# Optimization experiments

Measured on AMD Instinct MI355X. Metric: run time of the kernel, lower is better.

Reference implementation:

```python
import jax, jax.numpy as jnp
import numpy as np

N = 50000
E = 1600000
F_IN = 128
MP_UNITS = [32, 32, 32, 32, 16, 16, 16, 16, 8, 8, 8, 8]
MLP_UNITS = [16, 16]
DELTA = 2.0


def _lin(k, fi, fo):
    kw, kb = jax.random.split(k)
    s = 1.0 / np.sqrt(fi)
    W = jax.random.uniform(kw, (fi, fo), minval=-s, maxval=s, dtype=jnp.float32)
    b = jax.random.uniform(kb, (fo,), minval=-s, maxval=s, dtype=jnp.float32)
    return W, b


def setup_inputs() -> dict:
    key = jax.random.key(0)
    ks = jax.random.split(key, 64)
    inp = {}
    inp['x'] = jax.random.normal(ks[0], (N, F_IN), dtype=jnp.float32)
    inp['edge_index'] = jax.random.randint(ks[1], (2, E), 0, N, dtype=jnp.int32)
    inp['edge_weight'] = jax.random.uniform(ks[2], (E,), dtype=jnp.float32)
    inp['Wi'], inp['bi'] = _lin(ks[3], F_IN, F_IN)
    d = F_IN
    for i, u in enumerate(MP_UNITS):
        inp['Wc%d' % i], inp['bc%d' % i] = _lin(ks[4 + i], d, u)
        d = u
    for i, u in enumerate(MLP_UNITS):
        inp['Wm%d' % i], inp['bm%d' % i] = _lin(ks[20 + i], d, u)
        d = u
    inp['Wf'], inp['bf'] = _lin(ks[30], d, 1)
    return inp


def reference(x, edge_index, edge_weight, Wi, bi,
              Wc0, bc0, Wc1, bc1, Wc2, bc2, Wc3, bc3, Wc4, bc4, Wc5, bc5,
              Wc6, bc6, Wc7, bc7, Wc8, bc8, Wc9, bc9, Wc10, bc10, Wc11, bc11,
              Wm0, bm0, Wm1, bm1, Wf, bf):
    n = x.shape[0]
    src, dst = edge_index[0], edge_index[1]
    # delta_gcn_matrix: P = (1-delta) I + delta * D^{-1/2} A D^{-1/2}
    deg = jax.ops.segment_sum(edge_weight, dst, num_segments=n)
    dinv = jnp.where(deg > 0, jax.lax.rsqrt(jnp.maximum(deg, 1e-12)), 0.0)
    w = DELTA * dinv[src] * edge_weight * dinv[dst]  # [E]
    self_w = 1.0 - DELTA

    h = x @ Wi + bi

    def conv(h, W, b):
        hw = h @ W                                        # [N, out]
        msg = hw[src] * w[:, None]                        # gather + scale [E, out]
        agg = jax.ops.segment_sum(msg, dst, num_segments=n)  # scatter-add
        return agg + self_w * hw + b                      # fold in self-loops

    convs = [(Wc0, bc0), (Wc1, bc1), (Wc2, bc2), (Wc3, bc3), (Wc4, bc4), (Wc5, bc5),
             (Wc6, bc6), (Wc7, bc7), (Wc8, bc8), (Wc9, bc9), (Wc10, bc10), (Wc11, bc11)]
    for W, b in convs:
        h = jnp.tanh(conv(h, W, b))
    for W, b in [(Wm0, bm0), (Wm1, bm1)]:
        h = jax.nn.relu(h @ W + b)
    return jnp.tanh(h @ Wf + bf)  # [N, 1]
```

## Files before the change

### kernel.cpp

```cpp
#include <hip/hip_runtime.h>


constexpr int kN = 50000;
constexpr int kE = 1600000;
constexpr float kSelfW = -1.0f;
constexpr int kCAP = 72;
constexpr int PAD_N = 50048;
constexpr int kPROWS = PAD_N / 8;
constexpr int E4  = kE / 4;
constexpr int E4B = (E4 + 255) / 256;
constexpr int NBG = (kN + 255) / 256;
constexpr int WSN = 50016;

typedef int      v4i __attribute__((ext_vector_type(4)));
typedef float    v4f __attribute__((ext_vector_type(4)));
typedef _Float16 h8v __attribute__((ext_vector_type(8)));

__device__ __forceinline__ int rowmap(int r) {
  return (r & 7) * kPROWS + (r >> 3);
}
__device__ __forceinline__ unsigned packcw(int col, float w) {
  _Float16 h = (_Float16)w;
  unsigned short u;
  __builtin_memcpy(&u, &h, 2);
  return (unsigned)(unsigned short)col | ((unsigned)u << 16);
}
__device__ __forceinline__ float unpw(unsigned e) {
  unsigned short u = (unsigned short)(e >> 16);
  _Float16 h;
  __builtin_memcpy(&h, &u, 2);
  return (float)h;
}
__device__ __forceinline__ unsigned pack2h(float a, float b) {
  _Float16 ha = (_Float16)a, hb = (_Float16)b;
  unsigned short ua, ub;
  __builtin_memcpy(&ua, &ha, 2);
  __builtin_memcpy(&ub, &hb, 2);
  return (unsigned)ua | ((unsigned)ub << 16);
}
__device__ __forceinline__ float fast_tanh(float x) {
  float t = __expf(2.0f * x);
  float r = __builtin_amdgcn_rcpf(t + 1.0f);
  return 1.0f - 2.0f * r;
}

__global__ __launch_bounds__(256)
void prep(int* __restrict__ cnt, const float* __restrict__ Wi,
          const float* __restrict__ bi, const float* __restrict__ Wc0,
          float* __restrict__ Weff, float* __restrict__ beff) {
  if (blockIdx.x < 49) {
    int i = blockIdx.x * 1024 + threadIdx.x * 4;
    if (i < PAD_N) *reinterpret_cast<int4*>(cnt + i) = make_int4(0, 0, 0, 0);
  } else {
    int idx = (blockIdx.x - 49) * 256 + threadIdx.x;
    if (idx >= 129 * 32) return;
    int r = idx >> 5, j = idx & 31;
    float acc = 0.0f;
    if (r < 128) {
      for (int k = 0; k < 128; ++k) acc += Wi[r * 128 + k] * Wc0[k * 32 + j];
      Weff[r * 32 + j] = acc;
    } else {
      for (int k = 0; k < 128; ++k) acc += bi[k] * Wc0[k * 32 + j];
      beff[j] = acc;
    }
  }
}

__global__ __launch_bounds__(256)
void cnt_rank_kernel(const int* __restrict__ dst, int* __restrict__ cnt,
                     int* __restrict__ rank, int e4) {
  int i = blockIdx.x * blockDim.x + threadIdx.x;
  if (i >= e4) return;
  int4 d = reinterpret_cast<const int4*>(dst)[i];
  int4 r;
  r.x = atomicAdd(&cnt[d.x], 1);
  r.y = atomicAdd(&cnt[d.y], 1);
  r.z = atomicAdd(&cnt[d.z], 1);
  r.w = atomicAdd(&cnt[d.w], 1);
  reinterpret_cast<int4*>(rank)[i] = r;
}

__global__ __launch_bounds__(256)
void gemm0(const float* __restrict__ X, const float* __restrict__ Weff,
           const float* __restrict__ beff, _Float16* __restrict__ Y, int n) {
  __shared__ float smem[4128];
  for (int idx = threadIdx.x; idx < 128 * 32; idx += 256) {
    int j = idx >> 7, k = idx & 127;
    smem[j * 128 + k] = Weff[k * 32 + j];
  }
  if (threadIdx.x < 32) smem[4096 + threadIdx.x] = beff[threadIdx.x];
  __syncthreads();
  int row = blockIdx.x * 256 + threadIdx.x;
  if (row >= n) return;
  float acc[32];
#pragma unroll
  for (int j = 0; j < 32; ++j) acc[j] = smem[4096 + j];
  const float4* xr = reinterpret_cast<const float4*>(X + (size_t)row * 128);
  const float4* Ws4 = reinterpret_cast<const float4*>(smem);
  for (int k4 = 0; k4 < 32; ++k4) {
    float4 a = xr[k4];
#pragma unroll
    for (int j = 0; j < 32; ++j) {
      float4 wv = Ws4[j * 32 + k4];
      acc[j] += a.x * wv.x + a.y * wv.y + a.z * wv.z + a.w * wv.w;
    }
  }
  h8v* yr = reinterpret_cast<h8v*>(Y + (size_t)row * 32);
#pragma unroll
  for (int j8 = 0; j8 < 4; ++j8) {
    h8v v;
#pragma unroll
    for (int q = 0; q < 8; ++q) v[q] = (_Float16)acc[8 * j8 + q];
    yr[j8] = v;
  }
}

__global__ __launch_bounds__(256)
void build_part(const int* __restrict__ src, const int* __restrict__ dst,
                const float* __restrict__ ew, const int* __restrict__ rank,
                unsigned* __restrict__ ecw, int e4) {
  int p = blockIdx.x & 7;
  int i = (blockIdx.x >> 3) * 256 + threadIdx.x;
  if (i >= e4) return;
  v4i sv = __builtin_nontemporal_load(reinterpret_cast<const v4i*>(src) + i);
  v4i dv = __builtin_nontemporal_load(reinterpret_cast<const v4i*>(dst) + i);
  v4i rv = __builtin_nontemporal_load(reinterpret_cast<const v4i*>(rank) + i);
  v4f wv = __builtin_nontemporal_load(reinterpret_cast<const v4f*>(ew) + i);
#pragma unroll
  for (int c = 0; c < 4; ++c) {
    int d = dv[c];
    if ((d & 7) == p) {
      int r = rv[c];
      if (r < kCAP)
        ecw[(size_t)(p * kPROWS + (d >> 3)) * kCAP + r] = packcw(sv[c], wv[c]);
    }
  }
}

__global__ __launch_bounds__(256)
void deg_dinv_wave(const int* __restrict__ cnt, const unsigned* __restrict__ ecw,
                   float* __restrict__ dinv, int n) {
  int lane = threadIdx.x & 63;
  int row = blockIdx.x * 4 + (threadIdx.x >> 6);
  int deg = min(cnt[row], kCAP);
  int base = rowmap(row) * kCAP;
  float d = 0.0f;
  for (int i = lane; i < deg; i += 64) d += unpw(ecw[base + i]);
#pragma unroll
  for (int off = 32; off > 0; off >>= 1) d += __shfl_xor(d, off, 64);
  if (lane == 0) dinv[row] = (d > 0.0f) ? rsqrtf(fmaxf(d, 1e-12f)) : 0.0f;
}

__global__ __launch_bounds__(256)
void wscale_wave(const int* __restrict__ cnt, unsigned* __restrict__ ecw,
                 const float* __restrict__ dinv, int n) {
  int lane = threadIdx.x & 63;
  int row = blockIdx.x * 4 + (threadIdx.x >> 6);
  if (row >= n) return;
  int deg = min(cnt[row], kCAP);
  int base = rowmap(row) * kCAP;
  float dr = 2.0f * dinv[row];
  for (int i = lane; i < kCAP; i += 64) {
    if (i < deg) {
      unsigned e = ecw[base + i];
      int col = e & 0xFFFFu;
      ecw[base + i] = packcw(col, dr * dinv[col] * unpw(e));
    } else {
      ecw[base + i] = 0u;
    }
  }
}

template <int DOUT, int DNEXT, bool FINAL>
__global__ __launch_bounds__(256)
void spmm_fused(const _Float16* __restrict__ HW, const int* __restrict__ cnt,
                const unsigned* __restrict__ ecw, const float* __restrict__ b,
                const float* __restrict__ Wn, void* __restrict__ Out,
                const float* __restrict__ Wm0, const float* __restrict__ bm0,
                const float* __restrict__ Wm1, const float* __restrict__ bm1,
                const float* __restrict__ Wf, const float* __restrict__ bf,
                int n) {
  constexpr int R = 64 / DOUT;
  constexpr int W = DOUT;
  constexpr int L = DOUT / 8;
  constexpr int S = 8;
  constexpr int WST = DNEXT + 1;
  constexpr int JPT = (DNEXT > 0) ? (DNEXT / S) : 1;
  __shared__ float smem[(DNEXT > 0) ? DOUT * WST : 448];
  if constexpr (DNEXT > 0) {
    for (int idx = threadIdx.x; idx < DOUT * DNEXT; idx += 256) {
      int k = idx / DNEXT, j = idx - k * DNEXT;
      smem[k * WST + j] = Wn[idx];
    }
    __syncthreads();
  }
  if constexpr (FINAL) {
    int t = threadIdx.x;
    if (t < 128) smem[t] = Wm0[t];
    if (t < 256) smem[128 + t] = Wm1[t];
    if (t < 16) {
      smem[384 + t] = bm0[t];
      smem[400 + t] = bm1[t];
      smem[416 + t] = Wf[t];
    }
    if (t == 0) smem[432] = bf[0];
    __syncthreads();
  }
  int lane = threadIdx.x & 63;
  int wid = threadIdx.x >> 6;
  int g = lane / W;
  int gl = lane - g * W;
  int ch8 = gl & (L - 1);
  int sub = gl / L;
  int row = (blockIdx.x * 4 + wid) * R + g;
  int deg = min(cnt[row], kCAP);
  const uint4* ecw4 = reinterpret_cast<const uint4*>(ecw + rowmap(row) * kCAP);
  const h8v* HW8 = reinterpret_cast<const h8v*>(HW);
  uint4 ea = ecw4[sub];
  uint4 eb = ecw4[8 + sub];
  h8v a0 = HW8[(size_t)(ea.x & 0xFFFFu) * L + ch8];
  h8v a1 = HW8[(size_t)(ea.y & 0xFFFFu) * L + ch8];
  h8v a2 = HW8[(size_t)(ea.z & 0xFFFFu) * L + ch8];
  h8v a3 = HW8[(size_t)(ea.w & 0xFFFFu) * L + ch8];
  h8v b0 = HW8[(size_t)(eb.x & 0xFFFFu) * L + ch8];
  h8v b1 = HW8[(size_t)(eb.y & 0xFFFFu) * L + ch8];
  h8v b2 = HW8[(size_t)(eb.z & 0xFFFFu) * L + ch8];
  h8v b3 = HW8[(size_t)(eb.w & 0xFFFFu) * L + ch8];
  float wa0 = unpw(ea.x), wa1 = unpw(ea.y), wa2 = unpw(ea.z), wa3 = unpw(ea.w);
  float wb0 = unpw(eb.x), wb1 = unpw(eb.y), wb2 = unpw(eb.z), wb3 = unpw(eb.w);
  float acc[8];
#pragma unroll
  for (int q = 0; q < 8; ++q)
    acc[q] = wa0 * (float)a0[q] + wa1 * (float)a1[q] +
             wa2 * (float)a2[q] + wa3 * (float)a3[q] +
             wb0 * (float)b0[q] + wb1 * (float)b1[q] +
             wb2 * (float)b2[q] + wb3 * (float)b3[q];
  if (deg > 64) {
    if (sub < 2) {
      uint4 et = ecw4[16 + sub];
      h8v t0 = HW8[(size_t)(et.x & 0xFFFFu) * L + ch8];
      h8v t1 = HW8[(size_t)(et.y & 0xFFFFu) * L + ch8];
      h8v t2 = HW8[(size_t)(et.z & 0xFFFFu) * L + ch8];
      h8v t3 = HW8[(size_t)(et.w & 0xFFFFu) * L + ch8];
      float u0 = unpw(et.x), u1 = unpw(et.y), u2 = unpw(et.z), u3 = unpw(et.w);
#pragma unroll
      for (int q = 0; q < 8; ++q)
        acc[q] += u0 * (float)t0[q] + u1 * (float)t1[q] +
                  u2 * (float)t2[q] + u3 * (float)t3[q];
    }
  }
#pragma unroll
  for (int off = W / 2; off >= L; off >>= 1) {
#pragma unroll
    for (int q = 0; q < 8; ++q) acc[q] += __shfl_xor(acc[q], off, 64);
  }
  int krow = 8 * ch8;
  h8v hsv = HW8[(size_t)row * L + ch8];
  float h[8];
#pragma unroll
  for (int q = 0; q < 8; ++q)
    h[q] = fast_tanh(acc[q] + kSelfW * (float)hsv[q] + b[krow + q]);
  if constexpr (FINAL) {
    if (gl == 0 && row < n) {
      float y0[16];
#pragma unroll
      for (int j = 0; j < 16; ++j) {
        float v = smem[384 + j];
#pragma unroll
        for (int k = 0; k < 8; ++k) v += h[k] * smem[k * 16 + j];
        y0[j] = fmaxf(v, 0.0f);
      }
      float y1[16];
#pragma unroll
      for (int j = 0; j < 16; ++j) {
        float v = smem[400 + j];
#pragma unroll
        for (int k = 0; k < 16; ++k) v += y0[k] * smem[128 + k * 16 + j];
        y1[j] = fmaxf(v, 0.0f);
      }
      float z = smem[432];
#pragma unroll
      for (int k = 0; k < 16; ++k) z += y1[k] * smem[416 + k];
      reinterpret_cast<float*>(Out)[row] = fast_tanh(z);
    }
  } else {
    float pj[JPT];
    int jbase = sub * JPT;
#pragma unroll
    for (int jj = 0; jj < JPT; ++jj) {
      int j = jbase + jj;
      float v = 0.0f;
#pragma unroll
      for (int q = 0; q < 8; ++q) v += h[q] * smem[(krow + q) * WST + j];
      pj[jj] = v;
    }
#pragma unroll
    for (int off = 1; off < L; off <<= 1) {
#pragma unroll
      for (int jj = 0; jj < JPT; ++jj) pj[jj] += __shfl_xor(pj[jj], off, 64);
    }
    if (ch8 == 0 && row < n) {
      _Float16* op = reinterpret_cast<_Float16*>(Out) + (size_t)row * DNEXT + jbase;
      if constexpr (JPT == 4) {
        uint2 u = make_uint2(pack2h(pj[0], pj[1]), pack2h(pj[2], pj[3]));
        *reinterpret_cast<uint2*>(op) = u;
      } else if constexpr (JPT == 2) {
        *reinterpret_cast<unsigned*>(op) = pack2h(pj[0], pj[1]);
      } else {
        op[0] = (_Float16)pj[0];
      }
    }
  }
}

extern "C" void kernel_launch(void* const* d_in, const int* in_sizes, int n_in,
                              void* d_out, int out_size, void* d_ws, size_t ws_size,
                              hipStream_t stream) {
  const float* x   = (const float*)d_in[0];
  const int*  eidx = (const int*)d_in[1];
  const float* ew  = (const float*)d_in[2];
  const float* Wi  = (const float*)d_in[3];
  const float* bi  = (const float*)d_in[4];
  const float* Wc[12]; const float* bc[12];
  for (int i = 0; i < 12; ++i) {
    Wc[i] = (const float*)d_in[5 + 2 * i];
    bc[i] = (const float*)d_in[6 + 2 * i];
  }
  const float* Wm0 = (const float*)d_in[29]; const float* bm0 = (const float*)d_in[30];
  const float* Wm1 = (const float*)d_in[31]; const float* bm1 = (const float*)d_in[32];
  const float* Wf  = (const float*)d_in[33]; const float* bf  = (const float*)d_in[34];
  float* out = (float*)d_out;

  const int* src = eidx;
  const int* dst = eidx + kE;

  float* wsf = (float*)d_ws;
  size_t off = 0;
  float*     dinv = wsf + off;              off += PAD_N;
  float*     Weff = wsf + off;              off += 128 * 32;
  float*     beff = wsf + off;              off += 64;
  int*       cnt  = (int*)(wsf + off);      off += PAD_N;
  unsigned*  ecw  = (unsigned*)(wsf + off); off += (size_t)PAD_N * kCAP;
  int*       rank = (int*)(wsf + off);      off += kE;
  _Float16*  B16  = (_Float16*)(wsf + off); off += (size_t)kN * 16;
  _Float16*  C16  = (_Float16*)(wsf + off); off += (size_t)kN * 16;

  const int dgb  = kN / 4;
  const int wsb  = WSN / 4;
  const int sb32 = kN / 8;
  const int sb16 = kN / 16;
  const int sb8  = (kN + 31) / 32;

  prep<<<66, 256, 0, stream>>>(cnt, Wi, bi, Wc[0], Weff, beff);
  cnt_rank_kernel<<<E4B, 256, 0, stream>>>(dst, cnt, rank, E4);
  gemm0<<<NBG, 256, 0, stream>>>(x, Weff, beff, B16, kN);
  build_part<<<E4B * 8, 256, 0, stream>>>(src, dst, ew, rank, ecw, E4);
  deg_dinv_wave<<<dgb, 256, 0, stream>>>(cnt, ecw, dinv, kN);
  wscale_wave<<<wsb, 256, 0, stream>>>(cnt, ecw, dinv, WSN);

  spmm_fused<32, 32, false><<<sb32, 256, 0, stream>>>(B16, cnt, ecw, bc[0], Wc[1], C16, nullptr, nullptr, nullptr, nullptr, nullptr, nullptr, kN);
  spmm_fused<32, 32, false><<<sb32, 256, 0, stream>>>(C16, cnt, ecw, bc[1], Wc[2], B16, nullptr, nullptr, nullptr, nullptr, nullptr, nullptr, kN);
  spmm_fused<32, 32, false><<<sb32, 256, 0, stream>>>(B16, cnt, ecw, bc[2], Wc[3], C16, nullptr, nullptr, nullptr, nullptr, nullptr, nullptr, kN);
  spmm_fused<32, 16, false><<<sb32, 256, 0, stream>>>(C16, cnt, ecw, bc[3], Wc[4], B16, nullptr, nullptr, nullptr, nullptr, nullptr, nullptr, kN);
  spmm_fused<16, 16, false><<<sb16, 256, 0, stream>>>(B16, cnt, ecw, bc[4], Wc[5], C16, nullptr, nullptr, nullptr, nullptr, nullptr, nullptr, kN);
  spmm_fused<16, 16, false><<<sb16, 256, 0, stream>>>(C16, cnt, ecw, bc[5], Wc[6], B16, nullptr, nullptr, nullptr, nullptr, nullptr, nullptr, kN);
  spmm_fused<16, 16, false><<<sb16, 256, 0, stream>>>(B16, cnt, ecw, bc[6], Wc[7], C16, nullptr, nullptr, nullptr, nullptr, nullptr, nullptr, kN);
  spmm_fused<16, 8, false><<<sb16, 256, 0, stream>>>(C16, cnt, ecw, bc[7], Wc[8], B16, nullptr, nullptr, nullptr, nullptr, nullptr, nullptr, kN);
  spmm_fused<8, 8, false><<<sb8, 256, 0, stream>>>(B16, cnt, ecw, bc[8], Wc[9], C16, nullptr, nullptr, nullptr, nullptr, nullptr, nullptr, kN);
  spmm_fused<8, 8, false><<<sb8, 256, 0, stream>>>(C16, cnt, ecw, bc[9], Wc[10], B16, nullptr, nullptr, nullptr, nullptr, nullptr, nullptr, kN);
  spmm_fused<8, 8, false><<<sb8, 256, 0, stream>>>(B16, cnt, ecw, bc[10], Wc[11], C16, nullptr, nullptr, nullptr, nullptr, nullptr, nullptr, kN);
  spmm_fused<8, 0, true><<<sb8, 256, 0, stream>>>(C16, cnt, ecw, bc[11], nullptr, out, Wm0, bm0, Wm1, bm1, Wf, bf, kN);
}
```

Baseline: 531.4 us.

## Store all node arrays in partition-permuted row order throughout pipeline

Counts, node features, the dinv vector and edge column indices now all use the rowmap permutation (row mod 8 partitions), and SpMM blocks iterate over the permuted rows directly. Each block's rows and ecw entries become contiguous, and the rowmap translation disappears from the hot kernels. PAD_N grows so the 8 partitions divide evenly, and padded rows are computed rather than bounds-checked. The risk is that gathers over source nodes now hit a permuted feature layout, which may change cache locality of the neighbor reads.

```diff
diff --git a/kernel.cpp b/kernel.cpp
--- a/kernel.cpp
+++ b/kernel.cpp
@@ -5,12 +5,11 @@
 constexpr int kE = 1600000;
 constexpr float kSelfW = -1.0f;
 constexpr int kCAP = 72;
-constexpr int PAD_N = 50048;
+constexpr int PAD_N = 50176;
 constexpr int kPROWS = PAD_N / 8;
 constexpr int E4  = kE / 4;
 constexpr int E4B = (E4 + 255) / 256;
 constexpr int NBG = (kN + 255) / 256;
-constexpr int WSN = 50016;
 
 typedef int      v4i __attribute__((ext_vector_type(4)));
 typedef float    v4f __attribute__((ext_vector_type(4)));
@@ -19,11 +18,11 @@
 __device__ __forceinline__ int rowmap(int r) {
   return (r & 7) * kPROWS + (r >> 3);
 }
-__device__ __forceinline__ unsigned packcw(int col, float w) {
+__device__ __forceinline__ unsigned packcw(int colMapped, float w) {
   _Float16 h = (_Float16)w;
   unsigned short u;
   __builtin_memcpy(&u, &h, 2);
-  return (unsigned)(unsigned short)col | ((unsigned)u << 16);
+  return (unsigned)(unsigned short)colMapped | ((unsigned)u << 16);
 }
 __device__ __forceinline__ float unpw(unsigned e) {
   unsigned short u = (unsigned short)(e >> 16);
@@ -50,7 +49,7 @@
           float* __restrict__ Weff, float* __restrict__ beff) {
   if (blockIdx.x < 49) {
     int i = blockIdx.x * 1024 + threadIdx.x * 4;
-    if (i < PAD_N) *reinterpret_cast<int4*>(cnt + i) = make_int4(0, 0, 0, 0);
+    *reinterpret_cast<int4*>(cnt + i) = make_int4(0, 0, 0, 0);
   } else {
     int idx = (blockIdx.x - 49) * 256 + threadIdx.x;
     if (idx >= 129 * 32) return;
@@ -73,10 +72,10 @@
   if (i >= e4) return;
   int4 d = reinterpret_cast<const int4*>(dst)[i];
   int4 r;
-  r.x = atomicAdd(&cnt[d.x], 1);
-  r.y = atomicAdd(&cnt[d.y], 1);
-  r.z = atomicAdd(&cnt[d.z], 1);
-  r.w = atomicAdd(&cnt[d.w], 1);
+  r.x = atomicAdd(&cnt[rowmap(d.x)], 1);
+  r.y = atomicAdd(&cnt[rowmap(d.y)], 1);
+  r.z = atomicAdd(&cnt[rowmap(d.z)], 1);
+  r.w = atomicAdd(&cnt[rowmap(d.w)], 1);
   reinterpret_cast<int4*>(rank)[i] = r;
 }
 
@@ -105,7 +104,7 @@
       acc[j] += a.x * wv.x + a.y * wv.y + a.z * wv.z + a.w * wv.w;
     }
   }
-  h8v* yr = reinterpret_cast<h8v*>(Y + (size_t)row * 32);
+  h8v* yr = reinterpret_cast<h8v*>(Y + (size_t)rowmap(row) * 32);
 #pragma unroll
   for (int j8 = 0; j8 < 4; ++j8) {
     h8v v;
@@ -132,39 +131,39 @@
     if ((d & 7) == p) {
       int r = rv[c];
       if (r < kCAP)
-        ecw[(size_t)(p * kPROWS + (d >> 3)) * kCAP + r] = packcw(sv[c], wv[c]);
+        ecw[(size_t)(p * kPROWS + (d >> 3)) * kCAP + r] =
+            packcw(rowmap(sv[c]), wv[c]);
     }
   }
 }
 
 __global__ __launch_bounds__(256)
 void deg_dinv_wave(const int* __restrict__ cnt, const unsigned* __restrict__ ecw,
-                   float* __restrict__ dinv, int n) {
+                   float* __restrict__ dinv) {
   int lane = threadIdx.x & 63;
-  int row = blockIdx.x * 4 + (threadIdx.x >> 6);
-  int deg = min(cnt[row], kCAP);
-  int base = rowmap(row) * kCAP;
+  int br = blockIdx.x * 4 + (threadIdx.x >> 6);
+  int deg = min(cnt[br], kCAP);
+  size_t base = (size_t)br * kCAP;
   float d = 0.0f;
   for (int i = lane; i < deg; i += 64) d += unpw(ecw[base + i]);
 #pragma unroll
   for (int off = 32; off > 0; off >>= 1) d += __shfl_xor(d, off, 64);
-  if (lane == 0) dinv[row] = (d > 0.0f) ? rsqrtf(fmaxf(d, 1e-12f)) : 0.0f;
+  if (lane == 0) dinv[br] = (d > 0.0f) ? rsqrtf(fmaxf(d, 1e-12f)) : 0.0f;
 }
 
 __global__ __launch_bounds__(256)
 void wscale_wave(const int* __restrict__ cnt, unsigned* __restrict__ ecw,
-                 const float* __restrict__ dinv, int n) {
+                 const float* __restrict__ dinv) {
   int lane = threadIdx.x & 63;
-  int row = blockIdx.x * 4 + (threadIdx.x >> 6);
-  if (row >= n) return;
-  int deg = min(cnt[row], kCAP);
-  int base = rowmap(row) * kCAP;
-  float dr = 2.0f * dinv[row];
+  int br = blockIdx.x * 4 + (threadIdx.x >> 6);
+  int deg = min(cnt[br], kCAP);
+  size_t base = (size_t)br * kCAP;
+  float dr = 2.0f * dinv[br];
   for (int i = lane; i < kCAP; i += 64) {
     if (i < deg) {
       unsigned e = ecw[base + i];
-      int col = e & 0xFFFFu;
-      ecw[base + i] = packcw(col, dr * dinv[col] * unpw(e));
+      int cm = e & 0xFFFFu;
+      ecw[base + i] = packcw(cm, dr * dinv[cm] * unpw(e));
     } else {
       ecw[base + i] = 0u;
     }
@@ -212,9 +211,12 @@
   int gl = lane - g * W;
   int ch8 = gl & (L - 1);
   int sub = gl / L;
-  int row = (blockIdx.x * 4 + wid) * R + g;
-  int deg = min(cnt[row], kCAP);
-  const uint4* ecw4 = reinterpret_cast<const uint4*>(ecw + rowmap(row) * kCAP);
+  int p = blockIdx.x & 7;
+  int q = blockIdx.x >> 3;
+  int brLocal = q * (4 * R) + wid * R + g;
+  int br = p * kPROWS + brLocal;
+  int deg = min(cnt[br], kCAP);
+  const uint4* ecw4 = reinterpret_cast<const uint4*>(ecw + (size_t)br * kCAP);
   const h8v* HW8 = reinterpret_cast<const h8v*>(HW);
   uint4 ea = ecw4[sub];
   uint4 eb = ecw4[8 + sub];
@@ -230,11 +232,11 @@
   float wb0 = unpw(eb.x), wb1 = unpw(eb.y), wb2 = unpw(eb.z), wb3 = unpw(eb.w);
   float acc[8];
 #pragma unroll
-  for (int q = 0; q < 8; ++q)
-    acc[q] = wa0 * (float)a0[q] + wa1 * (float)a1[q] +
-             wa2 * (float)a2[q] + wa3 * (float)a3[q] +
-             wb0 * (float)b0[q] + wb1 * (float)b1[q] +
-             wb2 * (float)b2[q] + wb3 * (float)b3[q];
+  for (int q8 = 0; q8 < 8; ++q8)
+    acc[q8] = wa0 * (float)a0[q8] + wa1 * (float)a1[q8] +
+              wa2 * (float)a2[q8] + wa3 * (float)a3[q8] +
+              wb0 * (float)b0[q8] + wb1 * (float)b1[q8] +
+              wb2 * (float)b2[q8] + wb3 * (float)b3[q8];
   if (deg > 64) {
     if (sub < 2) {
       uint4 et = ecw4[16 + sub];
@@ -244,23 +246,24 @@
       h8v t3 = HW8[(size_t)(et.w & 0xFFFFu) * L + ch8];
       float u0 = unpw(et.x), u1 = unpw(et.y), u2 = unpw(et.z), u3 = unpw(et.w);
 #pragma unroll
-      for (int q = 0; q < 8; ++q)
-        acc[q] += u0 * (float)t0[q] + u1 * (float)t1[q] +
-                  u2 * (float)t2[q] + u3 * (float)t3[q];
+      for (int q8 = 0; q8 < 8; ++q8)
+        acc[q8] += u0 * (float)t0[q8] + u1 * (float)t1[q8] +
+                   u2 * (float)t2[q8] + u3 * (float)t3[q8];
     }
   }
 #pragma unroll
   for (int off = W / 2; off >= L; off >>= 1) {
 #pragma unroll
-    for (int q = 0; q < 8; ++q) acc[q] += __shfl_xor(acc[q], off, 64);
+    for (int q8 = 0; q8 < 8; ++q8) acc[q8] += __shfl_xor(acc[q8], off, 64);
   }
   int krow = 8 * ch8;
-  h8v hsv = HW8[(size_t)row * L + ch8];
+  h8v hsv = HW8[(size_t)br * L + ch8];
   float h[8];
 #pragma unroll
-  for (int q = 0; q < 8; ++q)
-    h[q] = fast_tanh(acc[q] + kSelfW * (float)hsv[q] + b[krow + q]);
+  for (int q8 = 0; q8 < 8; ++q8)
+    h[q8] = fast_tanh(acc[q8] + kSelfW * (float)hsv[q8] + b[krow + q8]);
   if constexpr (FINAL) {
+    int row = (brLocal << 3) | p;
     if (gl == 0 && row < n) {
       float y0[16];
 #pragma unroll
@@ -291,7 +294,7 @@
       int j = jbase + jj;
       float v = 0.0f;
 #pragma unroll
-      for (int q = 0; q < 8; ++q) v += h[q] * smem[(krow + q) * WST + j];
+      for (int q8 = 0; q8 < 8; ++q8) v += h[q8] * smem[(krow + q8) * WST + j];
       pj[jj] = v;
     }
 #pragma unroll
@@ -299,8 +302,8 @@
 #pragma unroll
       for (int jj = 0; jj < JPT; ++jj) pj[jj] += __shfl_xor(pj[jj], off, 64);
     }
-    if (ch8 == 0 && row < n) {
-      _Float16* op = reinterpret_cast<_Float16*>(Out) + (size_t)row * DNEXT + jbase;
+    if (ch8 == 0) {
+      _Float16* op = reinterpret_cast<_Float16*>(Out) + (size_t)br * DNEXT + jbase;
       if constexpr (JPT == 4) {
         uint2 u = make_uint2(pack2h(pj[0], pj[1]), pack2h(pj[2], pj[3]));
         *reinterpret_cast<uint2*>(op) = u;
@@ -342,21 +345,20 @@
   int*       cnt  = (int*)(wsf + off);      off += PAD_N;
   unsigned*  ecw  = (unsigned*)(wsf + off); off += (size_t)PAD_N * kCAP;
   int*       rank = (int*)(wsf + off);      off += kE;
-  _Float16*  B16  = (_Float16*)(wsf + off); off += (size_t)kN * 16;
-  _Float16*  C16  = (_Float16*)(wsf + off); off += (size_t)kN * 16;
-
-  const int dgb  = kN / 4;
-  const int wsb  = WSN / 4;
-  const int sb32 = kN / 8;
-  const int sb16 = kN / 16;
-  const int sb8  = (kN + 31) / 32;
+  _Float16*  B16  = (_Float16*)(wsf + off); off += (size_t)PAD_N * 16;
+  _Float16*  C16  = (_Float16*)(wsf + off); off += (size_t)PAD_N * 16;
+
+  const int dgb  = PAD_N / 4;
+  const int sb32 = PAD_N / 8;
+  const int sb16 = PAD_N / 16;
+  const int sb8  = PAD_N / 32;
 
   prep<<<66, 256, 0, stream>>>(cnt, Wi, bi, Wc[0], Weff, beff);
   cnt_rank_kernel<<<E4B, 256, 0, stream>>>(dst, cnt, rank, E4);
   gemm0<<<NBG, 256, 0, stream>>>(x, Weff, beff, B16, kN);
   build_part<<<E4B * 8, 256, 0, stream>>>(src, dst, ew, rank, ecw, E4);
-  deg_dinv_wave<<<dgb, 256, 0, stream>>>(cnt, ecw, dinv, kN);
-  wscale_wave<<<wsb, 256, 0, stream>>>(cnt, ecw, dinv, WSN);
+  deg_dinv_wave<<<dgb, 256, 0, stream>>>(cnt, ecw, dinv);
+  wscale_wave<<<dgb, 256, 0, stream>>>(cnt, ecw, dinv);
 
   spmm_fused<32, 32, false><<<sb32, 256, 0, stream>>>(B16, cnt, ecw, bc[0], Wc[1], C16, nullptr, nullptr, nullptr, nullptr, nullptr, nullptr, kN);
   spmm_fused<32, 32, false><<<sb32, 256, 0, stream>>>(C16, cnt, ecw, bc[1], Wc[2], B16, nullptr, nullptr, nullptr, nullptr, nullptr, nullptr, kN);
```

After: 519.5 us, median of 2. 2.2% less time.
